# Kernel optimization log

Hardware: AMD Instinct MI355X
Metric: run time of the kernel (lower is better)

The kernel has to match this reference:

```python
import jax, jax.numpy as jnp
import numpy as np

N_QUBITS = 12
DIM = 2 ** N_QUBITS  # 4096
N_LAYERS = 3
N_LABELS = 28
B = 1024
IN_DIM = 768

# PennyLane default.qubit convention: wire 0 is the most-significant bit.
_idx = np.arange(DIM)
_bits = (_idx[:, None] >> (N_QUBITS - 1 - np.arange(N_QUBITS))) & 1
_Z = (1.0 - 2.0 * _bits).astype(np.float32)  # (DIM, 12): eigenvalues of Z_q per basis state
_ZZ = np.stack([_Z[:, i] * _Z[:, i + 1] for i in range(N_QUBITS - 1)], axis=1)  # (DIM, 11)


def _apply_1q(state, U, q):
    # state: (B, DIM) complex; U: (2,2) shared or (B,2,2) per-sample
    b = state.shape[0]
    left, right = 2 ** q, 2 ** (N_QUBITS - q - 1)
    s = state.reshape(b, left, 2, right)
    if U.ndim == 2:
        s = jnp.einsum('ab,kxbj->kxaj', U, s)
    else:
        s = jnp.einsum('kab,kxbj->kxaj', U, s)
    return s.reshape(b, DIM)


def _apply_cnot(state, c, t):
    b = state.shape[0]
    s = state.reshape((b,) + (2,) * N_QUBITS)
    s = jnp.moveaxis(s, (c + 1, t + 1), (-2, -1))
    # flip target amplitudes where control bit == 1
    s = jnp.stack([s[..., 0, :], s[..., 1, ::-1]], axis=-2)
    s = jnp.moveaxis(s, (-2, -1), (c + 1, t + 1))
    return s.reshape(b, DIM)


def _ry_mats(angles):
    # angles: (B, 12) -> (B, 12, 2, 2) complex RY matrices
    c, s = jnp.cos(angles / 2), jnp.sin(angles / 2)
    U = jnp.stack([jnp.stack([c, -s], -1), jnp.stack([s, c], -1)], -2)
    return U.astype(jnp.complex64)


def _rot_mats(w):
    # w: (12, 3) -> (12, 2, 2); qml.Rot(phi, theta, omega) = RZ(omega) RY(theta) RZ(phi)
    phi, theta, omega = w[:, 0], w[:, 1], w[:, 2]
    c = jnp.cos(theta / 2).astype(jnp.complex64)
    s = jnp.sin(theta / 2).astype(jnp.complex64)
    a = jnp.exp(-0.5j * (phi + omega)) * c
    bb = -jnp.exp(0.5j * (phi - omega)) * s
    cc = jnp.exp(-0.5j * (phi - omega)) * s
    d = jnp.exp(0.5j * (phi + omega)) * c
    return jnp.stack([jnp.stack([a, bb], -1), jnp.stack([cc, d], -1)], -2)


def _forward(x, W1, b1, ln_g, ln_b, W2, b2, qws, scales, biases):
    # --- DimensionalityReduction MLP (eval mode: dropout = identity) ---
    h = x @ W1.T + b1                                   # (B, 24)
    mu = h.mean(-1, keepdims=True)
    var = ((h - mu) ** 2).mean(-1, keepdims=True)
    h = (h - mu) / jnp.sqrt(var + 1e-5) * ln_g + ln_b   # LayerNorm
    h = jax.nn.relu(h)
    angles = jnp.tanh(h @ W2.T + b2)                    # (B, 12) in [-1, 1]

    # --- batched 12-qubit state-vector simulation ---
    state = jnp.zeros((angles.shape[0], DIM), jnp.complex64).at[:, 0].set(1.0)
    Ury = _ry_mats(angles)                              # (B, 12, 2, 2)
    for l in range(N_LAYERS):
        for q in range(N_QUBITS):                       # AngleEmbedding (RY, per sample)
            state = _apply_1q(state, Ury[:, q], q)
        R = _rot_mats(qws[l][0])                        # StronglyEntanglingLayers: Rot per qubit
        for q in range(N_QUBITS):
            state = _apply_1q(state, R[q], q)
        for q in range(N_QUBITS):                       # CNOT ring, range 1
            state = _apply_cnot(state, q, (q + 1) % N_QUBITS)

    probs = state.real ** 2 + state.imag ** 2           # (B, DIM)
    eZ = probs @ jnp.asarray(_Z)                        # (B, 12)
    eZZ = probs @ jnp.asarray(_ZZ)                      # (B, 11)
    eX = []
    for q in range(N_LABELS - N_QUBITS - (N_QUBITS - 1)):  # 5 PauliX observables
        left, right = 2 ** q, 2 ** (N_QUBITS - q - 1)
        s = state.reshape(-1, left, 2, right)
        eX.append(2 * jnp.sum(s[:, :, 0, :].real * s[:, :, 1, :].real
                              + s[:, :, 0, :].imag * s[:, :, 1, :].imag, axis=(1, 2)))
    exps = jnp.concatenate([eZ, eZZ, jnp.stack(eX, -1)], axis=1)  # (B, 28)
    return exps * scales + biases


def setup_inputs() -> dict:
    key = jax.random.key(0)
    ks = jax.random.split(key, 8)
    x = jax.random.normal(ks[0], (B, IN_DIM), jnp.float32)
    W1 = jax.random.normal(ks[1], (2 * N_QUBITS, IN_DIM), jnp.float32) * 0.05
    b1 = jnp.zeros((2 * N_QUBITS,), jnp.float32)
    ln_g = jnp.ones((2 * N_QUBITS,), jnp.float32)
    ln_b = jnp.zeros((2 * N_QUBITS,), jnp.float32)
    W2 = jax.random.normal(ks[2], (N_QUBITS, 2 * N_QUBITS), jnp.float32) * 0.2
    b2 = jnp.zeros((N_QUBITS,), jnp.float32)
    qw0 = jax.random.normal(ks[3], (1, N_QUBITS, 3), jnp.float32) * 0.1
    qw1 = jax.random.normal(ks[4], (1, N_QUBITS, 3), jnp.float32) * 0.1
    qw2 = jax.random.normal(ks[5], (1, N_QUBITS, 3), jnp.float32) * 0.1
    scales = jnp.ones((N_LABELS,), jnp.float32)
    biases = jnp.zeros((N_LABELS,), jnp.float32)
    return {"x": x, "W1": W1, "b1": b1, "ln_g": ln_g, "ln_b": ln_b, "W2": W2,
            "b2": b2, "qw0": qw0, "qw1": qw1, "qw2": qw2,
            "scales": scales, "biases": biases}


def reference(x, W1, b1, ln_g, ln_b, W2, b2, qw0, qw1, qw2, scales, biases):
    return _forward(x, W1, b1, ln_g, ln_b, W2, b2, (qw0, qw1, qw2), scales, biases)
```

## Files before the change

### kernel.cpp

```cpp
#include <hip/hip_runtime.h>
#include <math.h>

#define NQ   12
#define BLK  256
#define IND  768
#define HD   24
#define NOBS 28
#define CSTR 20

typedef float    f32x2 __attribute__((ext_vector_type(2)));
typedef float    f32x4 __attribute__((ext_vector_type(4)));
typedef __fp16   f16x2 __attribute__((ext_vector_type(2)));
typedef _Float16 h8    __attribute__((ext_vector_type(8)));

__device__ __forceinline__ unsigned pkrtz(float x, float y) {
    f16x2 h = __builtin_amdgcn_cvt_pkrtz(x, y);
    unsigned u; __builtin_memcpy(&u, &h, 4); return u;
}
__device__ __forceinline__ f32x2 unpack2(unsigned u) {
    f16x2 h; __builtin_memcpy(&h, &u, 4);
    f32x2 v; v.x = (float)h.x; v.y = (float)h.y; return v;
}
__device__ __forceinline__ f32x2 pk_cmul(f32x2 m, f32x2 u) {
    f32x2 r;
    asm("v_pk_mul_f32 %0, %1, %2 op_sel:[0,0] op_sel_hi:[0,1]"
        : "=v"(r) : "v"(m), "v"(u));
    asm("v_pk_fma_f32 %0, %1, %2, %0 op_sel:[1,1,0] op_sel_hi:[1,0,1] neg_lo:[0,1,0]"
        : "+v"(r) : "v"(m), "v"(u));
    return r;
}
__device__ __forceinline__ void pk_fma_plain(f32x2& acc, f32x2 a, f32x2 b) {
    asm("v_pk_fma_f32 %0, %1, %2, %0" : "+v"(acc) : "v"(a), "v"(b));
}
__device__ __forceinline__ h8 as_h8(uint4 u) { h8 r; __builtin_memcpy(&r, &u, 16); return r; }

__device__ __forceinline__ int pfx12(int y) { y ^= y >> 1; y ^= y >> 2; y ^= y >> 4; y ^= y >> 8; return y; }
__device__ __forceinline__ int pfx8 (int y) { y ^= y >> 1; y ^= y >> 2; y ^= y >> 4; return y; }

template<int LI, int G, int WM>
__device__ __forceinline__ void gstage(unsigned* st, const float GM[3][NQ][8],
                                       int l, int w) {
    const int a  = l & 15;
    const int mb = (l >> 4) * 4;

    unsigned A0u[4], A1u[4];
    #pragma unroll
    for (int bi = 0; bi < 4; ++bi) {
        const int bq = mb + bi;
        f32x2 u;
        {
            const float* F = GM[LI][11 - 4*G];
            const int off = (a & 1) * 4 + (bq & 1) * 2;
            u.x = F[off]; u.y = F[off + 1];
        }
        #pragma unroll
        for (int p = 1; p < 4; ++p) {
            const float* F = GM[LI][11 - 4*G - p];
            const int off = ((a >> p) & 1) * 4 + ((bq >> p) & 1) * 2;
            f32x2 e; e.x = F[off]; e.y = F[off + 1];
            u = pk_cmul(e, u);
        }
        A0u[bi] = pkrtz(u.x, -u.y);
        A1u[bi] = pkrtz(u.y,  u.x);
    }

    __syncthreads();
    uint4 Bf[4];
    #pragma unroll
    for (int tt = 0; tt < 4; ++tt)
        Bf[tt] = *(const uint4*)(st + (16 * (4*w + tt) + a) * CSTR + mb);
    __syncthreads();

    uint4 A04; A04.x = A0u[0]; A04.y = A0u[1]; A04.z = A0u[2]; A04.w = A0u[3];
    uint4 A14; A14.x = A1u[0]; A14.y = A1u[1]; A14.z = A1u[2]; A14.w = A1u[3];
    const h8 A0 = as_h8(A04), A1 = as_h8(A14);

    int TL = 0;
    if (WM >= 2) TL = pfx12(mb << 8);
    const int CTJ[4] = {0, 0x1FF, 0x3FF, 0x200};

    #pragma unroll
    for (int tt = 0; tt < 4; ++tt) {
        f32x4 c0 = {0.f, 0.f, 0.f, 0.f}, c1 = {0.f, 0.f, 0.f, 0.f};
        const h8 Bh = as_h8(Bf[tt]);
        c0 = __builtin_amdgcn_mfma_f32_16x16x32_f16(A0, Bh, c0, 0, 0, 0);
        c1 = __builtin_amdgcn_mfma_f32_16x16x32_f16(A1, Bh, c1, 0, 0, 0);
        const int n  = 16 * (4*w + tt) + a;
        const int TN = (WM >= 2) ? (pfx8(n) ^ TL) : 0;
        #pragma unroll
        for (int j = 0; j < 4; ++j) {
            const int m = mb + j;
            int addr;
            if (WM == 0)      addr = (m | (n & 0xF0)) * CSTR + (n & 15);
            else if (WM == 1) addr = ((n & 15) | (m << 4)) * CSTR + (n >> 4);
            else {
                const int tz = TN ^ CTJ[j];
                const int jp = tz ^ ((tz & 1) << 11);
                addr = (WM == 2) ? ((jp >> 4) * CSTR + (jp & 15))
                                 : ((jp & 255) * CSTR + (jp >> 8));
            }
            st[addr] = pkrtz(c0[j], c1[j]);
        }
    }
}

__global__ void __launch_bounds__(BLK) pqm_kernel(
    const float* __restrict__ x,   const float* __restrict__ W1,
    const float* __restrict__ b1,  const float* __restrict__ ln_g,
    const float* __restrict__ ln_b,const float* __restrict__ W2,
    const float* __restrict__ b2,  const float* __restrict__ qw0,
    const float* __restrict__ qw1, const float* __restrict__ qw2,
    const float* __restrict__ scales, const float* __restrict__ biases,
    float* __restrict__ out)
{
    __shared__ unsigned st[256 * CSTR];
    __shared__ float GM[3][NQ][8];
    __shared__ float hb[HD];
    __shared__ float ang[2 * NQ];
    __shared__ float wpar[4][24];

    const int t   = threadIdx.x;
    const int w   = t >> 6;
    const int l   = t & 63;
    const int row = blockIdx.x;

    float* xs = (float*)st;
    if (t < 192) ((float4*)xs)[t] = ((const float4*)(x + row * IND))[t];
    __syncthreads();

    {
        int g = t >> 3, l8 = t & 7;
        if (g < HD) {
            const float* wp = W1 + g * IND + l8 * 96;
            const float* xp = xs + l8 * 96;
            float acc = 0.f;
            #pragma unroll
            for (int j = 0; j < 24; ++j) {
                float4 w4 = *(const float4*)(wp + 4 * j);
                float4 a4 = *(const float4*)(xp + 4 * j);
                acc += a4.x * w4.x + a4.y * w4.y + a4.z * w4.z + a4.w * w4.w;
            }
            acc += __shfl_down(acc, 4, 8);
            acc += __shfl_down(acc, 2, 8);
            acc += __shfl_down(acc, 1, 8);
            if (l8 == 0) hb[g] = acc + b1[g];
        } else if (t >= 192 && t < 228) {
            int u = t - 192; int li = u / NQ, q = u % NQ;
            const float* qw = (li == 0) ? qw0 : ((li == 1) ? qw1 : qw2);
            float phi = qw[q*3+0], th = qw[q*3+1], om = qw[q*3+2];
            float c = cosf(0.5f*th), s = sinf(0.5f*th);
            float sp, cp, sm, cm;
            sincosf(0.5f*(phi+om), &sp, &cp);
            sincosf(0.5f*(phi-om), &sm, &cm);
            float* R = GM[li][q];
            R[0] =  cp*c;  R[1] = -sp*c;
            R[2] = -cm*s;  R[3] = -sm*s;
            R[4] =  cm*s;  R[5] = -sm*s;
            R[6] =  cp*c;  R[7] =  sp*c;
        }
    }
    __syncthreads();

    if (t < NQ) {
        float mu = 0.f;
        #pragma unroll
        for (int j = 0; j < HD; ++j) mu += hb[j];
        mu *= (1.f / HD);
        float var = 0.f;
        #pragma unroll
        for (int j = 0; j < HD; ++j) { float d = hb[j] - mu; var += d * d; }
        var *= (1.f / HD);
        float rinv = 1.f / sqrtf(var + 1e-5f);
        float acc = b2[t];
        #pragma unroll
        for (int j = 0; j < HD; ++j) {
            float hn = (hb[j] - mu) * rinv * ln_g[j] + ln_b[j];
            acc += fmaxf(hn, 0.f) * W2[t * HD + j];
        }
        float a = tanhf(acc);
        ang[t]      = cosf(0.5f * a);
        ang[NQ + t] = sinf(0.5f * a);
    }
    __syncthreads();
    if (t < 36) {
        int li = t / NQ, q = t % NQ;
        float* R = GM[li][q];
        float r0=R[0],r1=R[1],r2=R[2],r3=R[3],r4=R[4],r5=R[5],r6=R[6],r7=R[7];
        float cr = ang[q], sr = ang[NQ + q];
        R[0] =  r0*cr + r2*sr;  R[1] =  r1*cr + r3*sr;
        R[2] = -r0*sr + r2*cr;  R[3] = -r1*sr + r3*cr;
        R[4] =  r4*cr + r6*sr;  R[5] =  r5*cr + r7*sr;
        R[6] = -r4*sr + r6*cr;  R[7] = -r5*sr + r7*cr;
    }
    __syncthreads();

    {
        f32x2 v0[16];
        f32x2 lf; lf.x = 1.f; lf.y = 0.f;
        #pragma unroll
        for (int u = 0; u < 8; ++u) {
            const float* F = GM[0][7 - u];
            const int bit = (t >> u) & 1;
            f32x2 e; e.x = F[bit * 4]; e.y = F[bit * 4 + 1];
            lf = pk_cmul(e, lf);
        }
        {
            const float* F = GM[0][11];
            f32x2 e0; e0.x = F[0]; e0.y = F[1];
            f32x2 e1; e1.x = F[4]; e1.y = F[5];
            v0[0] = pk_cmul(e0, lf); v0[1] = pk_cmul(e1, lf);
        }
        #pragma unroll
        for (int b = 1; b < 4; ++b) {
            const float* F = GM[0][11 - b];
            f32x2 e0; e0.x = F[0]; e0.y = F[1];
            f32x2 e1; e1.x = F[4]; e1.y = F[5];
            #pragma unroll
            for (int r = 0; r < (1 << b); ++r) {
                v0[r | (1 << b)] = pk_cmul(e1, v0[r]);
                v0[r]            = pk_cmul(e0, v0[r]);
            }
        }
        const int TL = pfx12(t << 4);
        #pragma unroll
        for (int r = 0; r < 16; ++r) {
            const int tr = r ^ (r >> 1) ^ (r >> 2) ^ (r >> 3);
            const int tz = TL ^ tr;
            const int jp = tz ^ ((tz & 1) << 11);
            st[(jp >> 4) * CSTR + (jp & 15)] = pkrtz(v0[r].x, v0[r].y);
        }
    }

    gstage<1, 0, 0>(st, GM, l, w);
    gstage<1, 1, 1>(st, GM, l, w);
    gstage<1, 2, 2>(st, GM, l, w);
    gstage<2, 0, 0>(st, GM, l, w);
    gstage<2, 1, 1>(st, GM, l, w);
    gstage<2, 2, 3>(st, GM, l, w);
    __syncthreads();

    {
        f32x2 v[16];
        #pragma unroll
        for (int i = 0; i < 4; ++i) {
            uint4 raw = *(const uint4*)(st + t * CSTR + 4 * i);
            v[4*i+0] = unpack2(raw.x); v[4*i+1] = unpack2(raw.y);
            v[4*i+2] = unpack2(raw.z); v[4*i+3] = unpack2(raw.w);
        }
        float ex[5];
        #pragma unroll
        for (int q = 0; q < 4; ++q) {
            f32x2 acc; acc.x = 0.f; acc.y = 0.f;
            const int m = 8 >> q;
            #pragma unroll
            for (int r = 0; r < 16; ++r) pk_fma_plain(acc, v[r], v[r ^ m]);
            ex[q] = acc.x + acc.y;
        }
        {
            f32x2 acc; acc.x = 0.f; acc.y = 0.f;
            #pragma unroll
            for (int i = 0; i < 4; ++i) {
                uint4 raw = *(const uint4*)(st + (t ^ 0x80) * CSTR + 4 * i);
                f32x2 p0 = unpack2(raw.x), p1 = unpack2(raw.y);
                f32x2 p2 = unpack2(raw.z), p3 = unpack2(raw.w);
                pk_fma_plain(acc, v[4*i+0], p0); pk_fma_plain(acc, v[4*i+1], p1);
                pk_fma_plain(acc, v[4*i+2], p2); pk_fma_plain(acc, v[4*i+3], p3);
            }
            ex[4] = acc.x + acc.y;
        }

        float pr[16];
        #pragma unroll
        for (int r = 0; r < 16; ++r) pr[r] = v[r].x * v[r].x + v[r].y * v[r].y;
        #pragma unroll
        for (int lev = 0; lev < 4; ++lev) {
            const int m = 1 << lev;
            #pragma unroll
            for (int r = 0; r < 16; ++r)
                if (!(r & m)) { float A = pr[r], B = pr[r | m]; pr[r] = A + B; pr[r | m] = A - B; }
        }

        float ch = pr[0];
        #pragma unroll
        for (int lev = 0; lev < 6; ++lev) {
            float o = __shfl_xor(ch, 1 << lev, 64);
            ch = (l & (1 << lev)) ? (o - ch) : (ch + o);
        }
        auto wsum = [&](float s) {
            #pragma unroll
            for (int d = 1; d < 64; d <<= 1) s += __shfl_xor(s, d, 64);
            return s;
        };
        float W8 = wsum(pr[8]),  W4 = wsum(pr[4]), W2 = wsum(pr[2]), W1 = wsum(pr[1]);
        float WC = wsum(pr[12]), W6 = wsum(pr[6]), W3 = wsum(pr[3]);
        float e0 = wsum(ex[0]), e1 = wsum(ex[1]), e2 = wsum(ex[2]);
        float e3 = wsum(ex[3]), e4 = wsum(ex[4]);

        if      (l == 0) {
            wpar[w][0]  = ch;
            wpar[w][12] = W8; wpar[w][13] = W4; wpar[w][14] = W2; wpar[w][15] = W1;
            wpar[w][16] = WC; wpar[w][17] = W6; wpar[w][18] = W3;
            wpar[w][19] = e0; wpar[w][20] = e1; wpar[w][21] = e2;
            wpar[w][22] = e3; wpar[w][23] = e4;
        }
        else if (l == 32) wpar[w][1]  = ch;
        else if (l == 16) wpar[w][2]  = ch;
        else if (l == 8)  wpar[w][3]  = ch;
        else if (l == 4)  wpar[w][4]  = ch;
        else if (l == 2)  wpar[w][5]  = ch;
        else if (l == 1)  wpar[w][6]  = ch;
        else if (l == 48) wpar[w][7]  = ch;
        else if (l == 24) wpar[w][8]  = ch;
        else if (l == 12) wpar[w][9]  = ch;
        else if (l == 6)  wpar[w][10] = ch;
        else if (l == 3)  wpar[w][11] = ch;
    }
    __syncthreads();

    if (t < NOBS) {
        const int oslot[NOBS] = {12,13,14,15, 0,0,1,2,3,4,5,6,
                                 16,17,18,15,0,1,7,8,9,10,11,
                                 19,20,21,22,23};
        const int omw[NOBS]   = {0,0,0,0, 2,1,0,0,0,0,0,0,
                                 0,0,0,2,3,1,0,0,0,0,0,
                                 0,0,0,0,0};
        const int sl = oslot[t], mw = omw[t];
        float s = 0.f;
        #pragma unroll
        for (int g = 0; g < 4; ++g) {
            float p = wpar[g][sl];
            s += (__popc(g & mw) & 1) ? -p : p;
        }
        out[row * NOBS + t] = s * scales[t] + biases[t];
    }
}

extern "C" void kernel_launch(void* const* d_in, const int* in_sizes, int n_in,
                              void* d_out, int out_size, void* d_ws, size_t ws_size,
                              hipStream_t stream) {
    const int Bn = in_sizes[0] / IND;
    pqm_kernel<<<dim3(Bn), dim3(BLK), 0, stream>>>(
        (const float*)d_in[0], (const float*)d_in[1], (const float*)d_in[2],
        (const float*)d_in[3], (const float*)d_in[4], (const float*)d_in[5],
        (const float*)d_in[6], (const float*)d_in[7], (const float*)d_in[8],
        (const float*)d_in[9], (const float*)d_in[10], (const float*)d_in[11],
        (float*)d_out);
}
```

Measured before the change: 29.06 us.

## Double block size to 512 threads, halving per-thread state and MFMA tiles

Raises the block from 256 to 512 threads. Each thread now holds 8 amplitudes instead of 16, each wave does 2 MFMA tiles per gate stage instead of 4, and the W1 dot product is split across 16 lanes instead of 8. The measurement reduction is reworked to cover 8 waves, with the top-qubit parity moved into the wave-sign mask and the LDS row stride changed to 22. The aim is more parallelism and lower register pressure per thread, in exchange for more barrier participants, more cross-wave reduction work, and possible changes in occupancy from the launch bound of 4.

```diff
diff --git a/kernel.cpp b/kernel.cpp
--- a/kernel.cpp
+++ b/kernel.cpp
@@ -2,11 +2,11 @@
 #include <math.h>
 
 #define NQ   12
-#define BLK  256
+#define BLK  512
 #define IND  768
 #define HD   24
 #define NOBS 28
-#define CSTR 20
+#define CSTR 22
 
 typedef float    f32x2 __attribute__((ext_vector_type(2)));
 typedef float    f32x4 __attribute__((ext_vector_type(4)));
@@ -63,29 +63,32 @@
         A0u[bi] = pkrtz(u.x, -u.y);
         A1u[bi] = pkrtz(u.y,  u.x);
     }
-
-    __syncthreads();
-    uint4 Bf[4];
-    #pragma unroll
-    for (int tt = 0; tt < 4; ++tt)
-        Bf[tt] = *(const uint4*)(st + (16 * (4*w + tt) + a) * CSTR + mb);
-    __syncthreads();
-
     uint4 A04; A04.x = A0u[0]; A04.y = A0u[1]; A04.z = A0u[2]; A04.w = A0u[3];
     uint4 A14; A14.x = A1u[0]; A14.y = A1u[1]; A14.z = A1u[2]; A14.w = A1u[3];
     const h8 A0 = as_h8(A04), A1 = as_h8(A14);
 
+    __syncthreads();
+    uint2 B0[2], B1[2];
+    #pragma unroll
+    for (int tt = 0; tt < 2; ++tt) {
+        const int base = (16 * (2*w + tt) + a) * CSTR + mb;
+        B0[tt] = *(const uint2*)(st + base);
+        B1[tt] = *(const uint2*)(st + base + 2);
+    }
+    __syncthreads();
+
     int TL = 0;
     if (WM >= 2) TL = pfx12(mb << 8);
     const int CTJ[4] = {0, 0x1FF, 0x3FF, 0x200};
 
     #pragma unroll
-    for (int tt = 0; tt < 4; ++tt) {
+    for (int tt = 0; tt < 2; ++tt) {
+        uint4 b4; b4.x = B0[tt].x; b4.y = B0[tt].y; b4.z = B1[tt].x; b4.w = B1[tt].y;
         f32x4 c0 = {0.f, 0.f, 0.f, 0.f}, c1 = {0.f, 0.f, 0.f, 0.f};
-        const h8 Bh = as_h8(Bf[tt]);
+        const h8 Bh = as_h8(b4);
         c0 = __builtin_amdgcn_mfma_f32_16x16x32_f16(A0, Bh, c0, 0, 0, 0);
         c1 = __builtin_amdgcn_mfma_f32_16x16x32_f16(A1, Bh, c1, 0, 0, 0);
-        const int n  = 16 * (4*w + tt) + a;
+        const int n  = 16 * (2*w + tt) + a;
         const int TN = (WM >= 2) ? (pfx8(n) ^ TL) : 0;
         #pragma unroll
         for (int j = 0; j < 4; ++j) {
@@ -104,7 +107,7 @@
     }
 }
 
-__global__ void __launch_bounds__(BLK) pqm_kernel(
+__global__ void __launch_bounds__(BLK, 4) pqm_kernel(
     const float* __restrict__ x,   const float* __restrict__ W1,
     const float* __restrict__ b1,  const float* __restrict__ ln_g,
     const float* __restrict__ ln_b,const float* __restrict__ W2,
@@ -117,7 +120,7 @@
     __shared__ float GM[3][NQ][8];
     __shared__ float hb[HD];
     __shared__ float ang[2 * NQ];
-    __shared__ float wpar[4][24];
+    __shared__ float wpar[8][22];
 
     const int t   = threadIdx.x;
     const int w   = t >> 6;
@@ -129,23 +132,24 @@
     __syncthreads();
 
     {
-        int g = t >> 3, l8 = t & 7;
+        int g = t >> 4, l16 = t & 15;
         if (g < HD) {
-            const float* wp = W1 + g * IND + l8 * 96;
-            const float* xp = xs + l8 * 96;
+            const float* wp = W1 + g * IND;
             float acc = 0.f;
             #pragma unroll
-            for (int j = 0; j < 24; ++j) {
-                float4 w4 = *(const float4*)(wp + 4 * j);
-                float4 a4 = *(const float4*)(xp + 4 * j);
+            for (int k = 0; k < 12; ++k) {
+                const int f4 = l16 + 16 * k;
+                float4 a4 = ((const float4*)xs)[f4];
+                float4 w4 = *(const float4*)(wp + 4 * f4);
                 acc += a4.x * w4.x + a4.y * w4.y + a4.z * w4.z + a4.w * w4.w;
             }
-            acc += __shfl_down(acc, 4, 8);
-            acc += __shfl_down(acc, 2, 8);
-            acc += __shfl_down(acc, 1, 8);
-            if (l8 == 0) hb[g] = acc + b1[g];
-        } else if (t >= 192 && t < 228) {
-            int u = t - 192; int li = u / NQ, q = u % NQ;
+            acc += __shfl_down(acc, 8, 16);
+            acc += __shfl_down(acc, 4, 16);
+            acc += __shfl_down(acc, 2, 16);
+            acc += __shfl_down(acc, 1, 16);
+            if (l16 == 0) hb[g] = acc + b1[g];
+        } else if (t >= 448 && t < 484) {
+            int u = t - 448; int li = u / NQ, q = u % NQ;
             const float* qw = (li == 0) ? qw0 : ((li == 1) ? qw1 : qw2);
             float phi = qw[q*3+0], th = qw[q*3+1], om = qw[q*3+2];
             float c = cosf(0.5f*th), s = sinf(0.5f*th);
@@ -195,11 +199,11 @@
     __syncthreads();
 
     {
-        f32x2 v0[16];
+        f32x2 v0[8];
         f32x2 lf; lf.x = 1.f; lf.y = 0.f;
         #pragma unroll
-        for (int u = 0; u < 8; ++u) {
-            const float* F = GM[0][7 - u];
+        for (int u = 0; u < 9; ++u) {
+            const float* F = GM[0][8 - u];
             const int bit = (t >> u) & 1;
             f32x2 e; e.x = F[bit * 4]; e.y = F[bit * 4 + 1];
             lf = pk_cmul(e, lf);
@@ -211,7 +215,7 @@
             v0[0] = pk_cmul(e0, lf); v0[1] = pk_cmul(e1, lf);
         }
         #pragma unroll
-        for (int b = 1; b < 4; ++b) {
+        for (int b = 1; b < 3; ++b) {
             const float* F = GM[0][11 - b];
             f32x2 e0; e0.x = F[0]; e0.y = F[1];
             f32x2 e1; e1.x = F[4]; e1.y = F[5];
@@ -221,10 +225,10 @@
                 v0[r]            = pk_cmul(e0, v0[r]);
             }
         }
-        const int TL = pfx12(t << 4);
-        #pragma unroll
-        for (int r = 0; r < 16; ++r) {
-            const int tr = r ^ (r >> 1) ^ (r >> 2) ^ (r >> 3);
+        const int TL = pfx12(t << 3);
+        #pragma unroll
+        for (int r = 0; r < 8; ++r) {
+            const int tr = r ^ (r >> 1) ^ (r >> 2);
             const int tz = TL ^ tr;
             const int jp = tz ^ ((tz & 1) << 11);
             st[(jp >> 4) * CSTR + (jp & 15)] = pkrtz(v0[r].x, v0[r].y);
@@ -240,47 +244,58 @@
     __syncthreads();
 
     {
-        f32x2 v[16];
-        #pragma unroll
-        for (int i = 0; i < 4; ++i) {
-            uint4 raw = *(const uint4*)(st + t * CSTR + 4 * i);
-            v[4*i+0] = unpack2(raw.x); v[4*i+1] = unpack2(raw.y);
-            v[4*i+2] = unpack2(raw.z); v[4*i+3] = unpack2(raw.w);
+        const int R = t & 255, h = t >> 8;
+        const int rowb = R * CSTR + 8 * h;
+        f32x2 v[8];
+        #pragma unroll
+        for (int p = 0; p < 4; ++p) {
+            uint2 raw = *(const uint2*)(st + rowb + 2 * p);
+            v[2*p]   = unpack2(raw.x);
+            v[2*p+1] = unpack2(raw.y);
         }
         float ex[5];
         #pragma unroll
-        for (int q = 0; q < 4; ++q) {
+        for (int q = 1; q <= 3; ++q) {
             f32x2 acc; acc.x = 0.f; acc.y = 0.f;
             const int m = 8 >> q;
             #pragma unroll
-            for (int r = 0; r < 16; ++r) pk_fma_plain(acc, v[r], v[r ^ m]);
+            for (int r = 0; r < 8; ++r) pk_fma_plain(acc, v[r], v[r ^ m]);
             ex[q] = acc.x + acc.y;
         }
         {
             f32x2 acc; acc.x = 0.f; acc.y = 0.f;
-            #pragma unroll
-            for (int i = 0; i < 4; ++i) {
-                uint4 raw = *(const uint4*)(st + (t ^ 0x80) * CSTR + 4 * i);
-                f32x2 p0 = unpack2(raw.x), p1 = unpack2(raw.y);
-                f32x2 p2 = unpack2(raw.z), p3 = unpack2(raw.w);
-                pk_fma_plain(acc, v[4*i+0], p0); pk_fma_plain(acc, v[4*i+1], p1);
-                pk_fma_plain(acc, v[4*i+2], p2); pk_fma_plain(acc, v[4*i+3], p3);
+            const int pb = R * CSTR + 8 * (h ^ 1);
+            #pragma unroll
+            for (int p = 0; p < 4; ++p) {
+                uint2 raw = *(const uint2*)(st + pb + 2 * p);
+                pk_fma_plain(acc, v[2*p],   unpack2(raw.x));
+                pk_fma_plain(acc, v[2*p+1], unpack2(raw.y));
+            }
+            ex[0] = acc.x + acc.y;
+        }
+        {
+            f32x2 acc; acc.x = 0.f; acc.y = 0.f;
+            const int pb = (R ^ 128) * CSTR + 8 * h;
+            #pragma unroll
+            for (int p = 0; p < 4; ++p) {
+                uint2 raw = *(const uint2*)(st + pb + 2 * p);
+                pk_fma_plain(acc, v[2*p],   unpack2(raw.x));
+                pk_fma_plain(acc, v[2*p+1], unpack2(raw.y));
             }
             ex[4] = acc.x + acc.y;
         }
 
-        float pr[16];
-        #pragma unroll
-        for (int r = 0; r < 16; ++r) pr[r] = v[r].x * v[r].x + v[r].y * v[r].y;
-        #pragma unroll
-        for (int lev = 0; lev < 4; ++lev) {
+        #pragma unroll
+        for (int r = 0; r < 8; ++r) v[r].x = v[r].x * v[r].x + v[r].y * v[r].y;
+        #pragma unroll
+        for (int lev = 0; lev < 3; ++lev) {
             const int m = 1 << lev;
             #pragma unroll
-            for (int r = 0; r < 16; ++r)
-                if (!(r & m)) { float A = pr[r], B = pr[r | m]; pr[r] = A + B; pr[r | m] = A - B; }
-        }
-
-        float ch = pr[0];
+            for (int r = 0; r < 8; ++r)
+                if (!(r & m)) { float A = v[r].x, B = v[r | m].x; v[r].x = A + B; v[r | m].x = A - B; }
+        }
+
+        float ch = v[0].x;
         #pragma unroll
         for (int lev = 0; lev < 6; ++lev) {
             float o = __shfl_xor(ch, 1 << lev, 64);
@@ -291,17 +306,17 @@
             for (int d = 1; d < 64; d <<= 1) s += __shfl_xor(s, d, 64);
             return s;
         };
-        float W8 = wsum(pr[8]),  W4 = wsum(pr[4]), W2 = wsum(pr[2]), W1 = wsum(pr[1]);
-        float WC = wsum(pr[12]), W6 = wsum(pr[6]), W3 = wsum(pr[3]);
+        float W4 = wsum(v[4].x), W2 = wsum(v[2].x), W1s = wsum(v[1].x);
+        float W6 = wsum(v[6].x), W3 = wsum(v[3].x);
         float e0 = wsum(ex[0]), e1 = wsum(ex[1]), e2 = wsum(ex[2]);
         float e3 = wsum(ex[3]), e4 = wsum(ex[4]);
 
         if      (l == 0) {
             wpar[w][0]  = ch;
-            wpar[w][12] = W8; wpar[w][13] = W4; wpar[w][14] = W2; wpar[w][15] = W1;
-            wpar[w][16] = WC; wpar[w][17] = W6; wpar[w][18] = W3;
-            wpar[w][19] = e0; wpar[w][20] = e1; wpar[w][21] = e2;
-            wpar[w][22] = e3; wpar[w][23] = e4;
+            wpar[w][12] = W4;  wpar[w][13] = W2; wpar[w][14] = W1s;
+            wpar[w][15] = W6;  wpar[w][16] = W3;
+            wpar[w][17] = e0;  wpar[w][18] = e1; wpar[w][19] = e2;
+            wpar[w][20] = e3;  wpar[w][21] = e4;
         }
         else if (l == 32) wpar[w][1]  = ch;
         else if (l == 16) wpar[w][2]  = ch;
@@ -318,16 +333,16 @@
     __syncthreads();
 
     if (t < NOBS) {
-        const int oslot[NOBS] = {12,13,14,15, 0,0,1,2,3,4,5,6,
-                                 16,17,18,15,0,1,7,8,9,10,11,
-                                 19,20,21,22,23};
-        const int omw[NOBS]   = {0,0,0,0, 2,1,0,0,0,0,0,0,
-                                 0,0,0,2,3,1,0,0,0,0,0,
+        const int oslot[NOBS] = {0,12,13,14, 0,0, 1,2,3,4,5,6,
+                                 12,15,16,14, 0,1, 7,8,9,10,11,
+                                 17,18,19,20,21};
+        const int omw[NOBS]   = {4,0,0,0, 2,1, 0,0,0,0,0,0,
+                                 4,0,0,2, 3,1, 0,0,0,0,0,
                                  0,0,0,0,0};
         const int sl = oslot[t], mw = omw[t];
         float s = 0.f;
         #pragma unroll
-        for (int g = 0; g < 4; ++g) {
+        for (int g = 0; g < 8; ++g) {
             float p = wpar[g][sl];
             s += (__popc(g & mw) & 1) ? -p : p;
         }
```

After: 27.90 us. -4.0%, faster.
